# Kernel tuning notes

Hardware: AMD Instinct MI355X
Metric: run time of the kernel (lower is better)

Reference implementation:

```python
import jax, jax.numpy as jnp
import numpy as np
from jax import lax

CR = 16        # opt.cr (temporal dim)
HEADS = 4      # num_heads
DIM = 64       # dim == channel count c
B = 2          # true batch; input batch = B*CR
H = W = 128


def setup_inputs() -> dict:
    key = jax.random.key(0)
    k1, k2, k3, k4 = jax.random.split(key, 4)
    return {
        "x": jax.random.normal(k1, (B * CR, DIM, H, W), jnp.float32),
        "ln_weight": jnp.ones((DIM,), jnp.float32),
        "ln_bias": jnp.zeros((DIM,), jnp.float32),
        "qkv_w": jax.random.normal(k2, (3 * CR, CR), jnp.float32) * 0.05,   # 1x1 conv
        "dw_w": jax.random.normal(k3, (3 * CR, 1, 3, 3), jnp.float32) * 0.1,  # depthwise 3x3
        "proj_w": jax.random.normal(k4, (DIM, DIM), jnp.float32) * 0.05,   # 1x1 conv
        "temperature": jnp.ones((HEADS, 1, 1), jnp.float32),
    }


def reference(x, ln_weight, ln_bias, qkv_w, dw_w, proj_w, temperature):
    b, c, h, w = x.shape
    Bt = b // CR
    # WithBias LayerNorm over channel dim (per spatial location), eps=1e-5
    mu = jnp.mean(x, axis=1, keepdims=True)
    var = jnp.mean(jnp.square(x - mu), axis=1, keepdims=True)
    xn = (x - mu) / jnp.sqrt(var + 1e-5)
    xn = xn * ln_weight[None, :, None, None] + ln_bias[None, :, None, None]
    # (B*cr, c, h, w) -> (B, cr, c, h, w) -> (B*c, cr, h, w)
    x_in = xn.reshape(Bt, CR, c, h, w).transpose(0, 2, 1, 3, 4).reshape(Bt * c, CR, h, w)
    # 1x1 qkv conv (no bias)
    qkv = jnp.einsum('oc,bchw->bohw', qkv_w, x_in)
    # depthwise 3x3 conv, padding 1
    qkv = lax.conv_general_dilated(qkv, dw_w, (1, 1), 'SAME',
                                   feature_group_count=3 * CR,
                                   dimension_numbers=('NCHW', 'OIHW', 'NCHW'))
    q, k, v = jnp.split(qkv, 3, axis=1)
    ch = CR // HEADS  # per-head channel dim

    def heads(t):
        return t.reshape(Bt * c, HEADS, ch, h * w)

    def l2n(t):
        n = jnp.sqrt(jnp.sum(jnp.square(t), axis=-1, keepdims=True))
        return t / jnp.maximum(n, 1e-12)

    q, k, v = heads(q), heads(k), heads(v)
    q, k = l2n(q), l2n(k)
    # transposed (channel) attention: small ch x ch scores
    attn = jnp.einsum('bhcn,bhdn->bhcd', q, k) * temperature[None]
    attn = jax.nn.softmax(attn, axis=-1)
    out = jnp.einsum('bhcd,bhdn->bhcn', attn, v)  # (B*c, heads, ch, hw)
    # (B*c, cr, h, w) -> (B, c, cr, h, w) -> (B*cr, c, h, w)
    out = out.reshape(Bt * c, CR, h, w).reshape(Bt, c, CR, h, w)
    out = out.transpose(0, 2, 1, 3, 4).reshape(b, c, h, w)
    # 1x1 project_out
    return jnp.einsum('oc,bchw->bohw', proj_w, out)
```

## Files before the change

### kernel.cpp

```cpp
#include <hip/hip_runtime.h>
#include <hip/hip_fp16.h>

typedef _Float16 half8_t __attribute__((ext_vector_type(8)));
typedef float float4_t __attribute__((ext_vector_type(4)));

__device__ __forceinline__ float2 h2f2(unsigned int u) {
  return __half22float2(__builtin_bit_cast(__half2, u));
}
__device__ __forceinline__ unsigned int f2h2(float a, float b) {
  return __builtin_bit_cast(unsigned int, __floats2half2_rn(a, b));
}

#if __has_builtin(__builtin_amdgcn_fdot2)
typedef _Float16 h2v __attribute__((ext_vector_type(2)));
__device__ __forceinline__ float fdot2(unsigned int a, unsigned int b, float c) {
  return __builtin_amdgcn_fdot2(__builtin_bit_cast(h2v, a),
                                __builtin_bit_cast(h2v, b), c, false);
}
#else
__device__ __forceinline__ float fdot2(unsigned int a, unsigned int b, float c) {
  float2 fa = h2f2(a), fb = h2f2(b);
  return fmaf(fa.y, fb.y, fmaf(fa.x, fb.x, c));
}
#endif

__global__ __launch_bounds__(256) void k_stats(
    const float2* __restrict__ x2, float4* __restrict__ stats4,
    const float* __restrict__ qkvw, const float* __restrict__ dww,
    const float* __restrict__ projw, unsigned int* __restrict__ qkvpk,
    unsigned int* __restrict__ dwpk, unsigned int* __restrict__ projpk) {
  if (blockIdx.x >= 1024) {
    for (int t = threadIdx.x; t < 2648; t += 256) {
      if (t < 2048) {
        int o = t >> 5, c2 = t & 31;
        projpk[t] = f2h2(projw[(o << 6) + 2 * c2], projw[(o << 6) + 2 * c2 + 1]);
      } else if (t < 2432) {
        int i = t - 2048;
        int ch = i >> 3, tp = i & 7;
        qkvpk[i] = f2h2(qkvw[(ch << 4) + 2 * tp], qkvw[(ch << 4) + 2 * tp + 1]);
      } else {
        int i = t - 2432;
        int pl = i / 9, k = i - pl * 9;
        dwpk[i] = f2h2(dww[18 * pl + k], dww[18 * pl + 9 + k]);
      }
    }
    return;
  }
  int id = blockIdx.x * 256 + threadIdx.x;
  int bb = id >> 13;
  int jp = id & 8191;
  const float2* xp = x2 + ((size_t)bb << 19) + jp;
  float s0 = 0.f, q0 = 0.f, s1 = 0.f, q1 = 0.f;
#pragma unroll
  for (int ci = 0; ci < 64; ++ci) {
    float2 v = xp[(size_t)ci << 13];
    s0 += v.x; q0 = fmaf(v.x, v.x, q0);
    s1 += v.y; q1 = fmaf(v.y, v.y, q1);
  }
  float mu0 = s0 * (1.f / 64.f), mu1 = s1 * (1.f / 64.f);
  float4 r;
  r.x = mu0; r.y = rsqrtf(fmaf(-mu0, mu0, q0 * (1.f / 64.f)) + 1e-5f);
  r.z = mu1; r.w = rsqrtf(fmaf(-mu1, mu1, q1 * (1.f / 64.f)) + 1e-5f);
  stats4[id] = r;
}

__global__ __launch_bounds__(256) void k_xn(
    const float2* __restrict__ x2, const float4* __restrict__ stats4,
    const float* __restrict__ lnw, const float* __restrict__ lnb,
    unsigned int* __restrict__ xnw) {
  int bc = blockIdx.y, bt = bc >> 6, ci = bc & 63;
  int jp = blockIdx.x * 256 + threadIdx.x;
  float lw = lnw[ci], lb = lnb[ci];
  unsigned int w0[8], w1[8];
#pragma unroll
  for (int tp = 0; tp < 8; ++tp) {
    int bb0 = (bt << 4) + 2 * tp;
    float2 xa = x2[(((size_t)((bb0 << 6) + ci)) << 13) + jp];
    float2 xb = x2[(((size_t)(((bb0 + 1) << 6) + ci)) << 13) + jp];
    float4 sa = stats4[((size_t)bb0 << 13) + jp];
    float4 sb = stats4[((size_t)(bb0 + 1) << 13) + jp];
    w0[tp] = f2h2(fmaf((xa.x - sa.x) * sa.y, lw, lb),
                  fmaf((xb.x - sb.x) * sb.y, lw, lb));
    w1[tp] = f2h2(fmaf((xa.y - sa.z) * sa.w, lw, lb),
                  fmaf((xb.y - sb.z) * sb.w, lw, lb));
  }
  size_t base = (((size_t)bc << 14) + 2 * (size_t)jp) * 8;
  *reinterpret_cast<uint4*>(&xnw[base + 0]) = make_uint4(w0[0], w0[1], w0[2], w0[3]);
  *reinterpret_cast<uint4*>(&xnw[base + 4]) = make_uint4(w0[4], w0[5], w0[6], w0[7]);
  *reinterpret_cast<uint4*>(&xnw[base + 8]) = make_uint4(w1[0], w1[1], w1[2], w1[3]);
  *reinterpret_cast<uint4*>(&xnw[base + 12]) = make_uint4(w1[4], w1[5], w1[6], w1[7]);
}

__global__ __launch_bounds__(256) void k_fused(
    const unsigned int* __restrict__ xnw, const unsigned int* __restrict__ qkvpk,
    const unsigned int* __restrict__ dwpk, unsigned int* __restrict__ vbuf,
    float* __restrict__ Sacc, float* __restrict__ Nacc) {
  __shared__ unsigned int pre[8 * 612];
  __shared__ unsigned int qk[16 * 258];
  int tid = threadIdx.x;
  int bc = blockIdx.y;
  int tx0 = (blockIdx.x & 3) << 5;
  int ty0 = (blockIdx.x >> 2) << 4;
  int lane15 = tid & 15;
  int kg = (tid >> 4) & 3;
  int wv = tid >> 6;
  int iy = tid >> 4, jx = tid & 15;
  int dwbase = iy * 34 + 2 * jx;

  uint4 bfr[10];
#pragma unroll
  for (int i = 0; i < 10; ++i) {
    int hp = (wv + 4 * i) * 16 + lane15;
    int hy = hp / 34, hx = hp - hy * 34;
    int gy = ty0 + hy - 1, gx = tx0 + hx - 1;
    bool ok = (hp < 612) && ((unsigned)gy < 128u) && ((unsigned)gx < 128u);
    uint4 bw = make_uint4(0, 0, 0, 0);
    if (ok && kg < 2)
      bw = *reinterpret_cast<const uint4*>(
          &xnw[((size_t)bc << 17) + (size_t)((gy << 7) + gx) * 8 + 4 * kg]);
    bfr[i] = bw;
  }

  for (int m = 0; m < 3; ++m) {
    if (m > 0) {
      int pm = m - 1;
      {
        int combo = tid >> 3, pc = tid & 7;
        int hp_ = combo >> 4, cd = combo & 15, cc = cd >> 2, dd = cd & 3;
        const unsigned int* qrow = qk + (4 * hp_ + cc) * 258;
        const unsigned int* krow = qk + (8 + 4 * hp_ + dd) * 258;
        float s = 0.f;
#pragma unroll
        for (int i = 0; i < 16; ++i) {
          uint2 q2 = *reinterpret_cast<const uint2*>(&qrow[2 * pc + (i << 4)]);
          uint2 k2 = *reinterpret_cast<const uint2*>(&krow[2 * pc + (i << 4)]);
          s = fdot2(q2.x, k2.x, s);
          s = fdot2(q2.y, k2.y, s);
        }
        s += __shfl_xor(s, 1); s += __shfl_xor(s, 2); s += __shfl_xor(s, 4);
        if (pc == 0)
          atomicAdd(&Sacc[((bc << 2) + 2 * pm + hp_) * 16 + cc * 4 + dd], s);
      }
      {
        int row = tid >> 4, pc = tid & 15;
        const unsigned int* rp = qk + row * 258;
        float n = 0.f;
#pragma unroll
        for (int i = 0; i < 8; ++i) {
          uint2 v2 = *reinterpret_cast<const uint2*>(&rp[2 * pc + (i << 5)]);
          n = fdot2(v2.x, v2.x, n);
          n = fdot2(v2.y, v2.y, n);
        }
        n += __shfl_xor(n, 1); n += __shfl_xor(n, 2);
        n += __shfl_xor(n, 4); n += __shfl_xor(n, 8);
        if (pc == 0) {
          int g = (row < 8) ? (8 * pm + row) : (16 + 8 * pm + (row - 8));
          atomicAdd(&Nacc[(bc << 5) + g], n);
        }
      }
    }
    {
      int gch = (m < 2)
                    ? ((lane15 < 8) ? (8 * m + lane15) : (16 + 8 * m + (lane15 - 8)))
                    : (32 + lane15);
      uint4 aw = make_uint4(0, 0, 0, 0);
      if (kg < 2) aw = *reinterpret_cast<const uint4*>(&qkvpk[gch * 8 + 4 * kg]);
      half8_t af = __builtin_bit_cast(half8_t, aw);
      float4_t zz = {0.f, 0.f, 0.f, 0.f};
#pragma unroll
      for (int i = 0; i < 10; ++i) {
        int hp = (wv + 4 * i) * 16 + lane15;
        half8_t bf = __builtin_bit_cast(half8_t, bfr[i]);
        float4_t d = __builtin_amdgcn_mfma_f32_16x16x32_f16(af, bf, zz, 0, 0, 0);
        if (hp < 612) {
          pre[(2 * kg) * 612 + hp] = f2h2(d[0], d[1]);
          pre[(2 * kg + 1) * 612 + hp] = f2h2(d[2], d[3]);
        }
      }
    }
    __syncthreads();
    unsigned int vs0[8], vs1[8];
#pragma unroll
    for (int pl = 0; pl < 8; ++pl) {
      int gpl = (m < 2) ? ((pl < 4) ? (4 * m + pl) : (8 + 4 * m + (pl - 4)))
                        : (16 + pl);
      const unsigned int* wp = dwpk + gpl * 9;
      __half2 a0 = __floats2half2_rn(0.f, 0.f), a1 = a0;
      int base = pl * 612 + dwbase;
#pragma unroll
      for (int dy = 0; dy < 3; ++dy) {
        uint2 A = *reinterpret_cast<const uint2*>(&pre[base + dy * 34]);
        uint2 B = *reinterpret_cast<const uint2*>(&pre[base + dy * 34 + 2]);
        __half2 d0 = __builtin_bit_cast(__half2, A.x);
        __half2 d1 = __builtin_bit_cast(__half2, A.y);
        __half2 d2 = __builtin_bit_cast(__half2, B.x);
        __half2 d3 = __builtin_bit_cast(__half2, B.y);
        __half2 w0 = __builtin_bit_cast(__half2, wp[dy * 3 + 0]);
        __half2 w1 = __builtin_bit_cast(__half2, wp[dy * 3 + 1]);
        __half2 w2 = __builtin_bit_cast(__half2, wp[dy * 3 + 2]);
        a0 = __hfma2(w0, d0, a0); a0 = __hfma2(w1, d1, a0); a0 = __hfma2(w2, d2, a0);
        a1 = __hfma2(w0, d1, a1); a1 = __hfma2(w1, d2, a1); a1 = __hfma2(w2, d3, a1);
      }
      unsigned int u0 = __builtin_bit_cast(unsigned int, a0);
      unsigned int u1 = __builtin_bit_cast(unsigned int, a1);
      if (m < 2) {
        qk[(2 * pl) * 258 + tid]     = (u0 & 0xFFFFu) | (u1 << 16);
        qk[(2 * pl + 1) * 258 + tid] = (u0 >> 16) | (u1 & 0xFFFF0000u);
      } else {
        vs0[pl] = u0;
        vs1[pl] = u1;
      }
    }
    if (m < 2) {
      __syncthreads();
    } else {
      int px0 = ((ty0 + iy) << 7) + tx0 + 2 * jx;
#pragma unroll
      for (int hg = 0; hg < 4; ++hg) {
        size_t a = (((size_t)(bc * 4 + hg)) << 15) + (size_t)px0 * 2;
        *reinterpret_cast<uint4*>(&vbuf[a]) =
            make_uint4(vs0[2 * hg], vs0[2 * hg + 1], vs1[2 * hg], vs1[2 * hg + 1]);
      }
    }
  }
}

__global__ __launch_bounds__(256) void k_outproj(
    const unsigned int* __restrict__ vbuf, const float* __restrict__ Sacc,
    const float* __restrict__ Nacc, const float* __restrict__ temp,
    const unsigned int* __restrict__ projpk, float* __restrict__ out) {
  __shared__ unsigned int Yl[32 * 260];
  __shared__ unsigned int attn_l[128];
  int tid = threadIdx.x;
  int comb = blockIdx.y;
  int bt = comb >> 4, hd = (comb >> 2) & 3, c = comb & 3;
  int lane15 = tid & 15;
  int kg = (tid >> 4) & 3;
  int wv = tid >> 6;

  if (tid < 64) {
    int b = (bt << 6) + tid;
    float tp = temp[hd];
    float iq = 1.f / fmaxf(sqrtf(Nacc[(b << 5) + (hd << 2) + c]), 1e-12f);
    float l[4];
#pragma unroll
    for (int d = 0; d < 4; ++d) {
      float ik = 1.f / fmaxf(sqrtf(Nacc[(b << 5) + 16 + (hd << 2) + d]), 1e-12f);
      l[d] = Sacc[((b << 2) + hd) * 16 + c * 4 + d] * iq * ik * tp;
    }
    float mx = fmaxf(fmaxf(l[0], l[1]), fmaxf(l[2], l[3]));
    float e0 = expf(l[0] - mx), e1 = expf(l[1] - mx);
    float e2 = expf(l[2] - mx), e3 = expf(l[3] - mx);
    float inv = 1.f / (e0 + e1 + e2 + e3);
    attn_l[2 * tid] = f2h2(e0 * inv, e1 * inv);
    attn_l[2 * tid + 1] = f2h2(e2 * inv, e3 * inv);
  }
  __syncthreads();

  {
    int gpx = (blockIdx.x << 8) + tid;
    size_t vb = (((size_t)(bt * 256 + hd)) << 15) + (size_t)gpx * 2;
#pragma unroll
    for (int ci2 = 0; ci2 < 32; ++ci2) {
      uint2 A0 = *reinterpret_cast<const uint2*>(&vbuf[vb + ((size_t)(2 * ci2) << 17)]);
      uint2 A1 = *reinterpret_cast<const uint2*>(&vbuf[vb + ((size_t)(2 * ci2 + 1) << 17)]);
      uint4 aw = *reinterpret_cast<const uint4*>(&attn_l[4 * ci2]);
      float y0 = fdot2(A0.x, aw.x, fdot2(A0.y, aw.y, 0.f));
      float y1 = fdot2(A1.x, aw.z, fdot2(A1.y, aw.w, 0.f));
      Yl[ci2 * 260 + tid] = f2h2(y0, y1);
    }
  }
  __syncthreads();

  half8_t A0[4], A1[4];
#pragma unroll
  for (int ot = 0; ot < 4; ++ot) {
    A0[ot] = __builtin_bit_cast(
        half8_t, *reinterpret_cast<const uint4*>(
                     &projpk[(ot * 16 + lane15) * 32 + kg * 4]));
    A1[ot] = __builtin_bit_cast(
        half8_t, *reinterpret_cast<const uint4*>(
                     &projpk[(ot * 16 + lane15) * 32 + 16 + kg * 4]));
  }
  float4_t zz = {0.f, 0.f, 0.f, 0.f};
  size_t outbase = ((size_t)comb << 20) + (blockIdx.x << 8);
#pragma unroll
  for (int pt = 0; pt < 4; ++pt) {
    int pxl = wv * 64 + pt * 16 + lane15;
    unsigned int r0 = Yl[(kg * 4 + 0) * 260 + pxl];
    unsigned int r1 = Yl[(kg * 4 + 1) * 260 + pxl];
    unsigned int r2 = Yl[(kg * 4 + 2) * 260 + pxl];
    unsigned int r3 = Yl[(kg * 4 + 3) * 260 + pxl];
    half8_t B0 = __builtin_bit_cast(half8_t, make_uint4(r0, r1, r2, r3));
    unsigned int s0 = Yl[(16 + kg * 4 + 0) * 260 + pxl];
    unsigned int s1 = Yl[(16 + kg * 4 + 1) * 260 + pxl];
    unsigned int s2 = Yl[(16 + kg * 4 + 2) * 260 + pxl];
    unsigned int s3 = Yl[(16 + kg * 4 + 3) * 260 + pxl];
    half8_t B1 = __builtin_bit_cast(half8_t, make_uint4(s0, s1, s2, s3));
#pragma unroll
    for (int ot = 0; ot < 4; ++ot) {
      float4_t d = __builtin_amdgcn_mfma_f32_16x16x32_f16(A0[ot], B0, zz, 0, 0, 0);
      d = __builtin_amdgcn_mfma_f32_16x16x32_f16(A1[ot], B1, d, 0, 0, 0);
      int o0 = ot * 16 + kg * 4;
#pragma unroll
      for (int r = 0; r < 4; ++r)
        out[outbase + ((size_t)(o0 + r) << 14) + pxl] = d[r];
    }
  }
}

extern "C" void kernel_launch(void* const* d_in, const int* in_sizes, int n_in,
                              void* d_out, int out_size, void* d_ws, size_t ws_size,
                              hipStream_t stream) {
  const float* x = (const float*)d_in[0];
  const float* lnw = (const float*)d_in[1];
  const float* lnb = (const float*)d_in[2];
  const float* qkvw = (const float*)d_in[3];
  const float* dww = (const float*)d_in[4];
  const float* projw = (const float*)d_in[5];
  const float* temp = (const float*)d_in[6];
  float* out = (float*)d_out;

  unsigned int* xnw = (unsigned int*)d_ws;
  unsigned int* vbuf = xnw + (67108864ull / 4);
  char* tail = (char*)d_ws + 134217728ull;
  float4* stats4 = (float4*)tail;
  float* Sacc = (float*)(tail + 4194304ull);
  float* Nacc = Sacc + 8192;
  unsigned int* projpk = (unsigned int*)(Nacc + 4096);
  unsigned int* qkvpk = projpk + 2048;
  unsigned int* dwpk = qkvpk + 384;

  hipMemsetAsync(Sacc, 0, (8192 + 4096) * sizeof(float), stream);
  k_stats<<<dim3(1025), dim3(256), 0, stream>>>((const float2*)x, stats4, qkvw,
                                                dww, projw, qkvpk, dwpk, projpk);
  k_xn<<<dim3(32, 128), dim3(256), 0, stream>>>((const float2*)x, stats4, lnw,
                                                lnb, xnw);
  k_fused<<<dim3(32, 128), dim3(256), 0, stream>>>(xnw, qkvpk, dwpk, vbuf, Sacc,
                                                   Nacc);
  k_outproj<<<dim3(64, 32), dim3(256), 0, stream>>>(vbuf, Sacc, Nacc, temp,
                                                    projpk, out);
}
```

Before: 192.5 us.

## Fuse LayerNorm stats and normalize kernels; loop heads' channels inside outproj

The separate stats and normalize kernels become one kernel. Each thread computes LayerNorm statistics for all 16 timesteps of its pixel pair in registers, then rereads x to write the fp16 normalized layout, so the stats buffer round-trip and one launch go away. Zeroing of the accumulators moves into that kernel's extra block in place of the memset. The output-projection kernel now computes all four softmax rows per block and loops over them, sharing setup and the projection weights across four blocks' worth of work. The fused kernel launches only 66 blocks, which leaves most of the GPU idle for a bandwidth-bound pass. The outproj grid also shrinks to a quarter of its former size.

Result: slower. 245.1 us (+27.3%).

```diff
diff --git a/kernel.cpp b/kernel.cpp
--- a/kernel.cpp
+++ b/kernel.cpp
@@ -24,71 +24,73 @@
 }
 #endif
 
-__global__ __launch_bounds__(256) void k_stats(
-    const float2* __restrict__ x2, float4* __restrict__ stats4,
+__global__ __launch_bounds__(256) void k_statsxn(
+    const float2* __restrict__ x2, const float* __restrict__ lnw,
+    const float* __restrict__ lnb, unsigned int* __restrict__ xnw,
     const float* __restrict__ qkvw, const float* __restrict__ dww,
     const float* __restrict__ projw, unsigned int* __restrict__ qkvpk,
-    unsigned int* __restrict__ dwpk, unsigned int* __restrict__ projpk) {
-  if (blockIdx.x >= 1024) {
-    for (int t = threadIdx.x; t < 2648; t += 256) {
-      if (t < 2048) {
-        int o = t >> 5, c2 = t & 31;
-        projpk[t] = f2h2(projw[(o << 6) + 2 * c2], projw[(o << 6) + 2 * c2 + 1]);
-      } else if (t < 2432) {
-        int i = t - 2048;
-        int ch = i >> 3, tp = i & 7;
-        qkvpk[i] = f2h2(qkvw[(ch << 4) + 2 * tp], qkvw[(ch << 4) + 2 * tp + 1]);
-      } else {
-        int i = t - 2432;
-        int pl = i / 9, k = i - pl * 9;
-        dwpk[i] = f2h2(dww[18 * pl + k], dww[18 * pl + 9 + k]);
-      }
+    unsigned int* __restrict__ dwpk, unsigned int* __restrict__ projpk,
+    float* __restrict__ Sacc) {
+  int bt = blockIdx.y;
+  if (blockIdx.x >= 32) {
+    if (bt == 0) {
+      for (int t = threadIdx.x; t < 2648; t += 256) {
+        if (t < 2048) {
+          int o = t >> 5, c2 = t & 31;
+          projpk[t] = f2h2(projw[(o << 6) + 2 * c2], projw[(o << 6) + 2 * c2 + 1]);
+        } else if (t < 2432) {
+          int i = t - 2048;
+          int ch = i >> 3, tp = i & 7;
+          qkvpk[i] = f2h2(qkvw[(ch << 4) + 2 * tp], qkvw[(ch << 4) + 2 * tp + 1]);
+        } else {
+          int i = t - 2432;
+          int pl = i / 9, k = i - pl * 9;
+          dwpk[i] = f2h2(dww[18 * pl + k], dww[18 * pl + 9 + k]);
+        }
+      }
+      for (int t = threadIdx.x; t < 12288; t += 256) Sacc[t] = 0.f;
     }
     return;
   }
-  int id = blockIdx.x * 256 + threadIdx.x;
-  int bb = id >> 13;
-  int jp = id & 8191;
-  const float2* xp = x2 + ((size_t)bb << 19) + jp;
-  float s0 = 0.f, q0 = 0.f, s1 = 0.f, q1 = 0.f;
-#pragma unroll
+  int jp = (blockIdx.x << 8) + threadIdx.x;
+  const float2* xb = x2 + ((size_t)(bt * 16) << 19) + jp;
+  float s0[16], q0[16], s1[16], q1[16];
+#pragma unroll
+  for (int t = 0; t < 16; ++t) { s0[t] = 0.f; q0[t] = 0.f; s1[t] = 0.f; q1[t] = 0.f; }
   for (int ci = 0; ci < 64; ++ci) {
-    float2 v = xp[(size_t)ci << 13];
-    s0 += v.x; q0 = fmaf(v.x, v.x, q0);
-    s1 += v.y; q1 = fmaf(v.y, v.y, q1);
-  }
-  float mu0 = s0 * (1.f / 64.f), mu1 = s1 * (1.f / 64.f);
-  float4 r;
-  r.x = mu0; r.y = rsqrtf(fmaf(-mu0, mu0, q0 * (1.f / 64.f)) + 1e-5f);
-  r.z = mu1; r.w = rsqrtf(fmaf(-mu1, mu1, q1 * (1.f / 64.f)) + 1e-5f);
-  stats4[id] = r;
-}
-
-__global__ __launch_bounds__(256) void k_xn(
-    const float2* __restrict__ x2, const float4* __restrict__ stats4,
-    const float* __restrict__ lnw, const float* __restrict__ lnb,
-    unsigned int* __restrict__ xnw) {
-  int bc = blockIdx.y, bt = bc >> 6, ci = bc & 63;
-  int jp = blockIdx.x * 256 + threadIdx.x;
-  float lw = lnw[ci], lb = lnb[ci];
-  unsigned int w0[8], w1[8];
-#pragma unroll
-  for (int tp = 0; tp < 8; ++tp) {
-    int bb0 = (bt << 4) + 2 * tp;
-    float2 xa = x2[(((size_t)((bb0 << 6) + ci)) << 13) + jp];
-    float2 xb = x2[(((size_t)(((bb0 + 1) << 6) + ci)) << 13) + jp];
-    float4 sa = stats4[((size_t)bb0 << 13) + jp];
-    float4 sb = stats4[((size_t)(bb0 + 1) << 13) + jp];
-    w0[tp] = f2h2(fmaf((xa.x - sa.x) * sa.y, lw, lb),
-                  fmaf((xb.x - sb.x) * sb.y, lw, lb));
-    w1[tp] = f2h2(fmaf((xa.y - sa.z) * sa.w, lw, lb),
-                  fmaf((xb.y - sb.z) * sb.w, lw, lb));
-  }
-  size_t base = (((size_t)bc << 14) + 2 * (size_t)jp) * 8;
-  *reinterpret_cast<uint4*>(&xnw[base + 0]) = make_uint4(w0[0], w0[1], w0[2], w0[3]);
-  *reinterpret_cast<uint4*>(&xnw[base + 4]) = make_uint4(w0[4], w0[5], w0[6], w0[7]);
-  *reinterpret_cast<uint4*>(&xnw[base + 8]) = make_uint4(w1[0], w1[1], w1[2], w1[3]);
-  *reinterpret_cast<uint4*>(&xnw[base + 12]) = make_uint4(w1[4], w1[5], w1[6], w1[7]);
+#pragma unroll
+    for (int t = 0; t < 16; ++t) {
+      float2 v = xb[((size_t)t << 19) + ((size_t)ci << 13)];
+      s0[t] += v.x; q0[t] = fmaf(v.x, v.x, q0[t]);
+      s1[t] += v.y; q1[t] = fmaf(v.y, v.y, q1[t]);
+    }
+  }
+#pragma unroll
+  for (int t = 0; t < 16; ++t) {
+    float mu0 = s0[t] * (1.f / 64.f), mu1 = s1[t] * (1.f / 64.f);
+    float r0 = rsqrtf(fmaf(-mu0, mu0, q0[t] * (1.f / 64.f)) + 1e-5f);
+    float r1 = rsqrtf(fmaf(-mu1, mu1, q1[t] * (1.f / 64.f)) + 1e-5f);
+    s0[t] = mu0; q0[t] = r0; s1[t] = mu1; q1[t] = r1;
+  }
+  size_t obase = ((size_t)(bt * 64) << 17) + (size_t)(2 * jp) * 8;
+  for (int ci = 0; ci < 64; ++ci) {
+    float lw = lnw[ci], lb = lnb[ci];
+    unsigned int w0[8], w1[8];
+#pragma unroll
+    for (int tp = 0; tp < 8; ++tp) {
+      float2 va = xb[((size_t)(2 * tp) << 19) + ((size_t)ci << 13)];
+      float2 vb = xb[((size_t)(2 * tp + 1) << 19) + ((size_t)ci << 13)];
+      w0[tp] = f2h2(fmaf((va.x - s0[2 * tp]) * q0[2 * tp], lw, lb),
+                    fmaf((vb.x - s0[2 * tp + 1]) * q0[2 * tp + 1], lw, lb));
+      w1[tp] = f2h2(fmaf((va.y - s1[2 * tp]) * q1[2 * tp], lw, lb),
+                    fmaf((vb.y - s1[2 * tp + 1]) * q1[2 * tp + 1], lw, lb));
+    }
+    unsigned int* dst = xnw + obase + ((size_t)ci << 17);
+    *reinterpret_cast<uint4*>(dst + 0) = make_uint4(w0[0], w0[1], w0[2], w0[3]);
+    *reinterpret_cast<uint4*>(dst + 4) = make_uint4(w0[4], w0[5], w0[6], w0[7]);
+    *reinterpret_cast<uint4*>(dst + 8) = make_uint4(w1[0], w1[1], w1[2], w1[3]);
+    *reinterpret_cast<uint4*>(dst + 12) = make_uint4(w1[4], w1[5], w1[6], w1[7]);
+  }
 }
 
 __global__ __launch_bounds__(256) void k_fused(
@@ -230,16 +232,17 @@
     const float* __restrict__ Nacc, const float* __restrict__ temp,
     const unsigned int* __restrict__ projpk, float* __restrict__ out) {
   __shared__ unsigned int Yl[32 * 260];
-  __shared__ unsigned int attn_l[128];
+  __shared__ unsigned int attn_l[512];
   int tid = threadIdx.x;
   int comb = blockIdx.y;
-  int bt = comb >> 4, hd = (comb >> 2) & 3, c = comb & 3;
+  int bt = comb >> 2, hd = comb & 3;
   int lane15 = tid & 15;
   int kg = (tid >> 4) & 3;
   int wv = tid >> 6;
 
-  if (tid < 64) {
-    int b = (bt << 6) + tid;
+  {
+    int c = tid >> 6, ci = tid & 63;
+    int b = (bt << 6) + ci;
     float tp = temp[hd];
     float iq = 1.f / fmaxf(sqrtf(Nacc[(b << 5) + (hd << 2) + c]), 1e-12f);
     float l[4];
@@ -252,23 +255,8 @@
     float e0 = expf(l[0] - mx), e1 = expf(l[1] - mx);
     float e2 = expf(l[2] - mx), e3 = expf(l[3] - mx);
     float inv = 1.f / (e0 + e1 + e2 + e3);
-    attn_l[2 * tid] = f2h2(e0 * inv, e1 * inv);
-    attn_l[2 * tid + 1] = f2h2(e2 * inv, e3 * inv);
-  }
-  __syncthreads();
-
-  {
-    int gpx = (blockIdx.x << 8) + tid;
-    size_t vb = (((size_t)(bt * 256 + hd)) << 15) + (size_t)gpx * 2;
-#pragma unroll
-    for (int ci2 = 0; ci2 < 32; ++ci2) {
-      uint2 A0 = *reinterpret_cast<const uint2*>(&vbuf[vb + ((size_t)(2 * ci2) << 17)]);
-      uint2 A1 = *reinterpret_cast<const uint2*>(&vbuf[vb + ((size_t)(2 * ci2 + 1) << 17)]);
-      uint4 aw = *reinterpret_cast<const uint4*>(&attn_l[4 * ci2]);
-      float y0 = fdot2(A0.x, aw.x, fdot2(A0.y, aw.y, 0.f));
-      float y1 = fdot2(A1.x, aw.z, fdot2(A1.y, aw.w, 0.f));
-      Yl[ci2 * 260 + tid] = f2h2(y0, y1);
-    }
+    attn_l[c * 128 + 2 * ci] = f2h2(e0 * inv, e1 * inv);
+    attn_l[c * 128 + 2 * ci + 1] = f2h2(e2 * inv, e3 * inv);
   }
   __syncthreads();
 
@@ -283,29 +271,48 @@
                      &projpk[(ot * 16 + lane15) * 32 + 16 + kg * 4]));
   }
   float4_t zz = {0.f, 0.f, 0.f, 0.f};
-  size_t outbase = ((size_t)comb << 20) + (blockIdx.x << 8);
-#pragma unroll
-  for (int pt = 0; pt < 4; ++pt) {
-    int pxl = wv * 64 + pt * 16 + lane15;
-    unsigned int r0 = Yl[(kg * 4 + 0) * 260 + pxl];
-    unsigned int r1 = Yl[(kg * 4 + 1) * 260 + pxl];
-    unsigned int r2 = Yl[(kg * 4 + 2) * 260 + pxl];
-    unsigned int r3 = Yl[(kg * 4 + 3) * 260 + pxl];
-    half8_t B0 = __builtin_bit_cast(half8_t, make_uint4(r0, r1, r2, r3));
-    unsigned int s0 = Yl[(16 + kg * 4 + 0) * 260 + pxl];
-    unsigned int s1 = Yl[(16 + kg * 4 + 1) * 260 + pxl];
-    unsigned int s2 = Yl[(16 + kg * 4 + 2) * 260 + pxl];
-    unsigned int s3 = Yl[(16 + kg * 4 + 3) * 260 + pxl];
-    half8_t B1 = __builtin_bit_cast(half8_t, make_uint4(s0, s1, s2, s3));
-#pragma unroll
-    for (int ot = 0; ot < 4; ++ot) {
-      float4_t d = __builtin_amdgcn_mfma_f32_16x16x32_f16(A0[ot], B0, zz, 0, 0, 0);
-      d = __builtin_amdgcn_mfma_f32_16x16x32_f16(A1[ot], B1, d, 0, 0, 0);
-      int o0 = ot * 16 + kg * 4;
-#pragma unroll
-      for (int r = 0; r < 4; ++r)
-        out[outbase + ((size_t)(o0 + r) << 14) + pxl] = d[r];
-    }
+  int gpx = (blockIdx.x << 8) + tid;
+  size_t vb = (((size_t)(bt * 256 + hd)) << 15) + (size_t)gpx * 2;
+
+  for (int c = 0; c < 4; ++c) {
+    {
+      const unsigned int* al = attn_l + c * 128;
+#pragma unroll
+      for (int ci2 = 0; ci2 < 32; ++ci2) {
+        uint2 A0v = *reinterpret_cast<const uint2*>(&vbuf[vb + ((size_t)(2 * ci2) << 17)]);
+        uint2 A1v = *reinterpret_cast<const uint2*>(&vbuf[vb + ((size_t)(2 * ci2 + 1) << 17)]);
+        uint4 aw = *reinterpret_cast<const uint4*>(&al[4 * ci2]);
+        float y0 = fdot2(A0v.x, aw.x, fdot2(A0v.y, aw.y, 0.f));
+        float y1 = fdot2(A1v.x, aw.z, fdot2(A1v.y, aw.w, 0.f));
+        Yl[ci2 * 260 + tid] = f2h2(y0, y1);
+      }
+    }
+    __syncthreads();
+    size_t outbase = ((size_t)((bt << 4) + (hd << 2) + c) << 20) + (blockIdx.x << 8);
+#pragma unroll
+    for (int pt = 0; pt < 4; ++pt) {
+      int pxl = wv * 64 + pt * 16 + lane15;
+      unsigned int r0 = Yl[(kg * 4 + 0) * 260 + pxl];
+      unsigned int r1 = Yl[(kg * 4 + 1) * 260 + pxl];
+      unsigned int r2 = Yl[(kg * 4 + 2) * 260 + pxl];
+      unsigned int r3 = Yl[(kg * 4 + 3) * 260 + pxl];
+      half8_t B0 = __builtin_bit_cast(half8_t, make_uint4(r0, r1, r2, r3));
+      unsigned int s0 = Yl[(16 + kg * 4 + 0) * 260 + pxl];
+      unsigned int s1 = Yl[(16 + kg * 4 + 1) * 260 + pxl];
+      unsigned int s2 = Yl[(16 + kg * 4 + 2) * 260 + pxl];
+      unsigned int s3 = Yl[(16 + kg * 4 + 3) * 260 + pxl];
+      half8_t B1 = __builtin_bit_cast(half8_t, make_uint4(s0, s1, s2, s3));
+#pragma unroll
+      for (int ot = 0; ot < 4; ++ot) {
+        float4_t d = __builtin_amdgcn_mfma_f32_16x16x32_f16(A0[ot], B0, zz, 0, 0, 0);
+        d = __builtin_amdgcn_mfma_f32_16x16x32_f16(A1[ot], B1, d, 0, 0, 0);
+        int o0 = ot * 16 + kg * 4;
+#pragma unroll
+        for (int r = 0; r < 4; ++r)
+          out[outbase + ((size_t)(o0 + r) << 14) + pxl] = d[r];
+      }
+    }
+    __syncthreads();
   }
 }
 
@@ -324,20 +331,17 @@
   unsigned int* xnw = (unsigned int*)d_ws;
   unsigned int* vbuf = xnw + (67108864ull / 4);
   char* tail = (char*)d_ws + 134217728ull;
-  float4* stats4 = (float4*)tail;
-  float* Sacc = (float*)(tail + 4194304ull);
+  float* Sacc = (float*)tail;
   float* Nacc = Sacc + 8192;
   unsigned int* projpk = (unsigned int*)(Nacc + 4096);
   unsigned int* qkvpk = projpk + 2048;
   unsigned int* dwpk = qkvpk + 384;
 
-  hipMemsetAsync(Sacc, 0, (8192 + 4096) * sizeof(float), stream);
-  k_stats<<<dim3(1025), dim3(256), 0, stream>>>((const float2*)x, stats4, qkvw,
-                                                dww, projw, qkvpk, dwpk, projpk);
-  k_xn<<<dim3(32, 128), dim3(256), 0, stream>>>((const float2*)x, stats4, lnw,
-                                                lnb, xnw);
+  k_statsxn<<<dim3(33, 2), dim3(256), 0, stream>>>(
+      (const float2*)x, lnw, lnb, xnw, qkvw, dww, projw, qkvpk, dwpk, projpk,
+      Sacc);
   k_fused<<<dim3(32, 128), dim3(256), 0, stream>>>(xnw, qkvpk, dwpk, vbuf, Sacc,
                                                    Nacc);
-  k_outproj<<<dim3(64, 32), dim3(256), 0, stream>>>(vbuf, Sacc, Nacc, temp,
-                                                    projpk, out);
-}
+  k_outproj<<<dim3(64, 8), dim3(256), 0, stream>>>(vbuf, Sacc, Nacc, temp,
+                                                   projpk, out);
+}
```

## Merge per-channel outproj blocks and fold accumulator zeroing into stats kernel

Applied to the files above, without the earlier changes.

Each k_outproj block now handles all four output channels of a head, looping over c, instead of one block per channel. This cuts the grid from 32 to 8 rows and lets the projection weight fragments load once per block. The vbuf reads are repeated per c but should mostly hit in cache, and the extra syncthreads per iteration serialise the stages. The hipMemsetAsync of Sacc/Nacc is replaced by zeroing inside the extra k_stats block, removing one launch.

Result: faster. 179.9 us (median of 2 runs) (-6.5%).

```diff
diff --git a/kernel.cpp b/kernel.cpp
--- a/kernel.cpp
+++ b/kernel.cpp
@@ -28,7 +28,8 @@
     const float2* __restrict__ x2, float4* __restrict__ stats4,
     const float* __restrict__ qkvw, const float* __restrict__ dww,
     const float* __restrict__ projw, unsigned int* __restrict__ qkvpk,
-    unsigned int* __restrict__ dwpk, unsigned int* __restrict__ projpk) {
+    unsigned int* __restrict__ dwpk, unsigned int* __restrict__ projpk,
+    float* __restrict__ Sacc) {
   if (blockIdx.x >= 1024) {
     for (int t = threadIdx.x; t < 2648; t += 256) {
       if (t < 2048) {
@@ -44,6 +45,7 @@
         dwpk[i] = f2h2(dww[18 * pl + k], dww[18 * pl + 9 + k]);
       }
     }
+    for (int t = threadIdx.x; t < 12288; t += 256) Sacc[t] = 0.f;
     return;
   }
   int id = blockIdx.x * 256 + threadIdx.x;
@@ -230,16 +232,17 @@
     const float* __restrict__ Nacc, const float* __restrict__ temp,
     const unsigned int* __restrict__ projpk, float* __restrict__ out) {
   __shared__ unsigned int Yl[32 * 260];
-  __shared__ unsigned int attn_l[128];
+  __shared__ unsigned int attn_l[512];
   int tid = threadIdx.x;
   int comb = blockIdx.y;
-  int bt = comb >> 4, hd = (comb >> 2) & 3, c = comb & 3;
+  int bt = comb >> 2, hd = comb & 3;
   int lane15 = tid & 15;
   int kg = (tid >> 4) & 3;
   int wv = tid >> 6;
 
-  if (tid < 64) {
-    int b = (bt << 6) + tid;
+  {
+    int c = tid >> 6, ci = tid & 63;
+    int b = (bt << 6) + ci;
     float tp = temp[hd];
     float iq = 1.f / fmaxf(sqrtf(Nacc[(b << 5) + (hd << 2) + c]), 1e-12f);
     float l[4];
@@ -252,23 +255,8 @@
     float e0 = expf(l[0] - mx), e1 = expf(l[1] - mx);
     float e2 = expf(l[2] - mx), e3 = expf(l[3] - mx);
     float inv = 1.f / (e0 + e1 + e2 + e3);
-    attn_l[2 * tid] = f2h2(e0 * inv, e1 * inv);
-    attn_l[2 * tid + 1] = f2h2(e2 * inv, e3 * inv);
-  }
-  __syncthreads();
-
-  {
-    int gpx = (blockIdx.x << 8) + tid;
-    size_t vb = (((size_t)(bt * 256 + hd)) << 15) + (size_t)gpx * 2;
-#pragma unroll
-    for (int ci2 = 0; ci2 < 32; ++ci2) {
-      uint2 A0 = *reinterpret_cast<const uint2*>(&vbuf[vb + ((size_t)(2 * ci2) << 17)]);
-      uint2 A1 = *reinterpret_cast<const uint2*>(&vbuf[vb + ((size_t)(2 * ci2 + 1) << 17)]);
-      uint4 aw = *reinterpret_cast<const uint4*>(&attn_l[4 * ci2]);
-      float y0 = fdot2(A0.x, aw.x, fdot2(A0.y, aw.y, 0.f));
-      float y1 = fdot2(A1.x, aw.z, fdot2(A1.y, aw.w, 0.f));
-      Yl[ci2 * 260 + tid] = f2h2(y0, y1);
-    }
+    attn_l[c * 128 + 2 * ci] = f2h2(e0 * inv, e1 * inv);
+    attn_l[c * 128 + 2 * ci + 1] = f2h2(e2 * inv, e3 * inv);
   }
   __syncthreads();
 
@@ -283,29 +271,48 @@
                      &projpk[(ot * 16 + lane15) * 32 + 16 + kg * 4]));
   }
   float4_t zz = {0.f, 0.f, 0.f, 0.f};
-  size_t outbase = ((size_t)comb << 20) + (blockIdx.x << 8);
-#pragma unroll
-  for (int pt = 0; pt < 4; ++pt) {
-    int pxl = wv * 64 + pt * 16 + lane15;
-    unsigned int r0 = Yl[(kg * 4 + 0) * 260 + pxl];
-    unsigned int r1 = Yl[(kg * 4 + 1) * 260 + pxl];
-    unsigned int r2 = Yl[(kg * 4 + 2) * 260 + pxl];
-    unsigned int r3 = Yl[(kg * 4 + 3) * 260 + pxl];
-    half8_t B0 = __builtin_bit_cast(half8_t, make_uint4(r0, r1, r2, r3));
-    unsigned int s0 = Yl[(16 + kg * 4 + 0) * 260 + pxl];
-    unsigned int s1 = Yl[(16 + kg * 4 + 1) * 260 + pxl];
-    unsigned int s2 = Yl[(16 + kg * 4 + 2) * 260 + pxl];
-    unsigned int s3 = Yl[(16 + kg * 4 + 3) * 260 + pxl];
-    half8_t B1 = __builtin_bit_cast(half8_t, make_uint4(s0, s1, s2, s3));
-#pragma unroll
-    for (int ot = 0; ot < 4; ++ot) {
-      float4_t d = __builtin_amdgcn_mfma_f32_16x16x32_f16(A0[ot], B0, zz, 0, 0, 0);
-      d = __builtin_amdgcn_mfma_f32_16x16x32_f16(A1[ot], B1, d, 0, 0, 0);
-      int o0 = ot * 16 + kg * 4;
-#pragma unroll
-      for (int r = 0; r < 4; ++r)
-        out[outbase + ((size_t)(o0 + r) << 14) + pxl] = d[r];
-    }
+  int gpx = (blockIdx.x << 8) + tid;
+  size_t vb = (((size_t)(bt * 256 + hd)) << 15) + (size_t)gpx * 2;
+
+  for (int c = 0; c < 4; ++c) {
+    {
+      const unsigned int* al = attn_l + c * 128;
+#pragma unroll
+      for (int ci2 = 0; ci2 < 32; ++ci2) {
+        uint2 A0v = *reinterpret_cast<const uint2*>(&vbuf[vb + ((size_t)(2 * ci2) << 17)]);
+        uint2 A1v = *reinterpret_cast<const uint2*>(&vbuf[vb + ((size_t)(2 * ci2 + 1) << 17)]);
+        uint4 aw = *reinterpret_cast<const uint4*>(&al[4 * ci2]);
+        float y0 = fdot2(A0v.x, aw.x, fdot2(A0v.y, aw.y, 0.f));
+        float y1 = fdot2(A1v.x, aw.z, fdot2(A1v.y, aw.w, 0.f));
+        Yl[ci2 * 260 + tid] = f2h2(y0, y1);
+      }
+    }
+    __syncthreads();
+    size_t outbase = ((size_t)((bt << 4) + (hd << 2) + c) << 20) + (blockIdx.x << 8);
+#pragma unroll
+    for (int pt = 0; pt < 4; ++pt) {
+      int pxl = wv * 64 + pt * 16 + lane15;
+      unsigned int r0 = Yl[(kg * 4 + 0) * 260 + pxl];
+      unsigned int r1 = Yl[(kg * 4 + 1) * 260 + pxl];
+      unsigned int r2 = Yl[(kg * 4 + 2) * 260 + pxl];
+      unsigned int r3 = Yl[(kg * 4 + 3) * 260 + pxl];
+      half8_t B0 = __builtin_bit_cast(half8_t, make_uint4(r0, r1, r2, r3));
+      unsigned int s0 = Yl[(16 + kg * 4 + 0) * 260 + pxl];
+      unsigned int s1 = Yl[(16 + kg * 4 + 1) * 260 + pxl];
+      unsigned int s2 = Yl[(16 + kg * 4 + 2) * 260 + pxl];
+      unsigned int s3 = Yl[(16 + kg * 4 + 3) * 260 + pxl];
+      half8_t B1 = __builtin_bit_cast(half8_t, make_uint4(s0, s1, s2, s3));
+#pragma unroll
+      for (int ot = 0; ot < 4; ++ot) {
+        float4_t d = __builtin_amdgcn_mfma_f32_16x16x32_f16(A0[ot], B0, zz, 0, 0, 0);
+        d = __builtin_amdgcn_mfma_f32_16x16x32_f16(A1[ot], B1, d, 0, 0, 0);
+        int o0 = ot * 16 + kg * 4;
+#pragma unroll
+        for (int r = 0; r < 4; ++r)
+          out[outbase + ((size_t)(o0 + r) << 14) + pxl] = d[r];
+      }
+    }
+    __syncthreads();
   }
 }
 
@@ -331,13 +338,13 @@
   unsigned int* qkvpk = projpk + 2048;
   unsigned int* dwpk = qkvpk + 384;
 
-  hipMemsetAsync(Sacc, 0, (8192 + 4096) * sizeof(float), stream);
   k_stats<<<dim3(1025), dim3(256), 0, stream>>>((const float2*)x, stats4, qkvw,
-                                                dww, projw, qkvpk, dwpk, projpk);
+                                                dww, projw, qkvpk, dwpk, projpk,
+                                                Sacc);
   k_xn<<<dim3(32, 128), dim3(256), 0, stream>>>((const float2*)x, stats4, lnw,
                                                 lnb, xnw);
   k_fused<<<dim3(32, 128), dim3(256), 0, stream>>>(xnw, qkvpk, dwpk, vbuf, Sacc,
                                                    Nacc);
-  k_outproj<<<dim3(64, 32), dim3(256), 0, stream>>>(vbuf, Sacc, Nacc, temp,
-                                                    projpk, out);
-}
+  k_outproj<<<dim3(64, 8), dim3(256), 0, stream>>>(vbuf, Sacc, Nacc, temp,
+                                                   projpk, out);
+}
```
